# Performance work log

Measured on AMD Instinct MI355X. Metric: run time of the kernel, lower is better.

Reference implementation:

```python
import jax, jax.numpy as jnp
import numpy as np

N = 50000        # nodes
E = 600000       # edges
F_IN = 128       # num_node_features
H = 128          # hidden_channels
G = 2000         # number of graphs (batch segments)
C = 1            # num_classes
EPS = 1e-5       # BatchNorm eps


def setup_inputs() -> dict:
    key = jax.random.key(0)
    ks = jax.random.split(key, 12)
    x = jax.random.normal(ks[0], (N, F_IN), dtype=jnp.float32)
    edge_index = jax.random.randint(ks[1], (2, E), 0, N, dtype=jnp.int32)
    batch = jnp.sort(jax.random.randint(ks[2], (N,), 0, G, dtype=jnp.int32))
    s = 0.05
    W1 = jax.random.normal(ks[3], (F_IN, H), dtype=jnp.float32) * s
    b1 = jnp.zeros((H,), dtype=jnp.float32)
    W2 = jax.random.normal(ks[4], (H, H), dtype=jnp.float32) * s
    b2 = jnp.zeros((H,), dtype=jnp.float32)
    W3 = jax.random.normal(ks[5], (H, H), dtype=jnp.float32) * s
    b3 = jnp.zeros((H,), dtype=jnp.float32)
    # BatchNorm (eval mode): running stats + affine params, stacked [3, H]
    bn_gamma = jnp.ones((3, H), dtype=jnp.float32)
    bn_beta = jnp.zeros((3, H), dtype=jnp.float32)
    bn_mean = jnp.zeros((3, H), dtype=jnp.float32)
    bn_var = jnp.ones((3, H), dtype=jnp.float32)
    lin1_W = jax.random.normal(ks[6], (3 * H, H), dtype=jnp.float32) * s
    lin1_b = jnp.zeros((H,), dtype=jnp.float32)
    lin2_W = jax.random.normal(ks[7], (H, C), dtype=jnp.float32) * s
    lin2_b = jnp.zeros((C,), dtype=jnp.float32)
    return {"x": x, "edge_index": edge_index, "batch": batch,
            "W1": W1, "b1": b1, "W2": W2, "b2": b2, "W3": W3, "b3": b3,
            "bn_gamma": bn_gamma, "bn_beta": bn_beta, "bn_mean": bn_mean, "bn_var": bn_var,
            "lin1_W": lin1_W, "lin1_b": lin1_b, "lin2_W": lin2_W, "lin2_b": lin2_b}


def _gcn_norm(edge_index):
    # Add self loops, compute symmetric normalization D^-1/2 (A+I) D^-1/2.
    loop = jnp.arange(N, dtype=edge_index.dtype)
    row = jnp.concatenate([edge_index[0], loop])   # sources (E+N,)
    col = jnp.concatenate([edge_index[1], loop])   # targets (E+N,)
    deg = jax.ops.segment_sum(jnp.ones(E + N, dtype=jnp.float32), col, num_segments=N)
    dinv = jnp.where(deg > 0, jax.lax.rsqrt(deg), 0.0)
    norm = dinv[row] * dinv[col]                   # (E+N,)
    return row, col, norm


def _gcn_conv(h, W, b, row, col, norm):
    h = h @ W                                      # [N, H] transform first (PyG GCNConv)
    msg = h[row] * norm[:, None]                   # edge-wise gather + scale
    out = jax.ops.segment_sum(msg, col, num_segments=N)  # scatter-add aggregate
    return out + b


def _bn_relu(h, g, b, m, v):
    return jax.nn.relu((h - m) * jax.lax.rsqrt(v + EPS) * g + b)


def reference(x, edge_index, batch, W1, b1, W2, b2, W3, b3,
              bn_gamma, bn_beta, bn_mean, bn_var,
              lin1_W, lin1_b, lin2_W, lin2_b):
    row, col, norm = _gcn_norm(edge_index)
    h = _bn_relu(_gcn_conv(x, W1, b1, row, col, norm), bn_gamma[0], bn_beta[0], bn_mean[0], bn_var[0])
    h = _bn_relu(_gcn_conv(h, W2, b2, row, col, norm), bn_gamma[1], bn_beta[1], bn_mean[1], bn_var[1])
    h = _bn_relu(_gcn_conv(h, W3, b3, row, col, norm), bn_gamma[2], bn_beta[2], bn_mean[2], bn_var[2])
    # Multi-pool over ragged graph segments
    seg = batch
    x_sum = jax.ops.segment_sum(h, seg, num_segments=G)                 # [G, H]
    cnt = jax.ops.segment_sum(jnp.ones((N,), dtype=h.dtype), seg, num_segments=G)
    x_mean = x_sum / jnp.maximum(cnt, 1.0)[:, None]
    x_max = jax.ops.segment_max(h, seg, num_segments=G)
    x_max = jnp.where(jnp.isfinite(x_max), x_max, 0.0)                  # empty segments -> 0
    z = jnp.concatenate([x_mean, x_max, x_sum], axis=1)                 # [G, 3H]
    z = jax.nn.relu(z @ lin1_W + lin1_b)
    return z @ lin2_W + lin2_b                                          # [G, C]
```

## Files before the change

kernel.cpp:

```cpp
#include <hip/hip_runtime.h>
#include <cfloat>
#include <cstdint>

#define N_NODES 50000
#define N_EDGES 600000
#define HDIM    128
#define NGRAPH  2000
#define BN_EPS  1e-5f


__global__ void k_init(int* degi, int* seg_s, int* seg_e) {
    int i = blockIdx.x * 256 + threadIdx.x;
    if (i < N_NODES) degi[i] = 1;
    if (i < NGRAPH) { seg_s[i] = 0x7FFFFFFF; seg_e[i] = 0; }
}

__global__ void k_count(const int* __restrict__ ei, int* degi) {
    int e = blockIdx.x * 256 + threadIdx.x;
    if (e < N_EDGES) atomicAdd(&degi[ei[N_EDGES + e]], 1);
}

__global__ void k_scanA(const int* __restrict__ degi, int* ptr, int* bsum, float* dinv) {
    __shared__ int t[256];
    int i = blockIdx.x * 256 + threadIdx.x;
    int v = (i < N_NODES) ? degi[i] : 0;
    if (i < N_NODES) dinv[i] = rsqrtf((float)v);
    t[threadIdx.x] = v; __syncthreads();
    for (int off = 1; off < 256; off <<= 1) {
        int a = (threadIdx.x >= off) ? t[threadIdx.x - off] : 0;
        __syncthreads();
        t[threadIdx.x] += a;
        __syncthreads();
    }
    if (i < N_NODES) ptr[i + 1] = t[threadIdx.x];
    if (threadIdx.x == 255) bsum[blockIdx.x] = t[255];
}

__global__ void k_scanB(const int* __restrict__ bsum, int* boff, int nb) {
    __shared__ int t[256];
    int i = threadIdx.x;
    int v = (i < nb) ? bsum[i] : 0;
    t[i] = v; __syncthreads();
    for (int off = 1; off < 256; off <<= 1) {
        int a = (i >= off) ? t[i - off] : 0;
        __syncthreads();
        t[i] += a;
        __syncthreads();
    }
    if (i < nb) boff[i] = t[i] - v;
}

__global__ void k_scanC(int* ptr, const int* __restrict__ boff, int* cursor) {
    int i = blockIdx.x * 256 + threadIdx.x;
    if (i < N_NODES) {
        int val = ptr[i + 1] + boff[blockIdx.x];
        ptr[i + 1] = val;
        if (i + 1 < N_NODES) cursor[i + 1] = val;
    }
    if (i == 0) { ptr[0] = 0; cursor[0] = 0; }
}

__global__ void k_fill(const int* __restrict__ ei, const float* __restrict__ dinv,
                       int* cursor, int2* meta) {
    int e = blockIdx.x * 256 + threadIdx.x;
    if (e < N_EDGES) {
        int r = ei[e], c = ei[N_EDGES + e];
        int pos = atomicAdd(&cursor[c], 1);
        meta[pos] = make_int2(r, __float_as_int(dinv[r] * dinv[c]));
    } else if (e < N_EDGES + N_NODES) {
        int v = e - N_EDGES;
        int pos = atomicAdd(&cursor[v], 1);
        float d = dinv[v];
        meta[pos] = make_int2(v, __float_as_int(d * d));
    }
}

__global__ void k_seg(const int* __restrict__ batch, int* seg_s, int* seg_e) {
    int i = blockIdx.x * 256 + threadIdx.x;
    if (i < N_NODES) {
        int g = batch[i];
        atomicMin(&seg_s[g], i);
        atomicMax(&seg_e[g], i + 1);
    }
}


__global__ __launch_bounds__(256) void k_layer(const float4* __restrict__ h4,
                                               const int* __restrict__ ptr,
                                               const int2* __restrict__ meta,
                                               const float4* __restrict__ W4,
                                               const float4* __restrict__ bias4,
                                               const float4* __restrict__ bng4,
                                               const float4* __restrict__ bnb4,
                                               const float4* __restrict__ bnm4,
                                               const float4* __restrict__ bnv4,
                                               float4* __restrict__ hout4) {
    __shared__ float4 Hs[32 * 32];
    int base = blockIdx.x * 32;
    int c = threadIdx.x & 31;
    int grp = threadIdx.x >> 5;

#pragma unroll
    for (int pass = 0; pass < 4; pass++) {
        int ln = pass * 8 + grp;
        int v = base + ln;
        if (v < N_NODES) {
            int e0 = ptr[v], e1 = ptr[v + 1];
            float ax = 0.f, ay = 0.f, az = 0.f, aw = 0.f;
            int j = e0;
            for (; j + 8 <= e1; j += 8) {
                int2 m[8];
#pragma unroll
                for (int i = 0; i < 8; i++) m[i] = meta[j + i];
                float4 vv[8];
#pragma unroll
                for (int i = 0; i < 8; i++) vv[i] = h4[(size_t)m[i].x * 32 + c];
#pragma unroll
                for (int i = 0; i < 8; i++) {
                    float n = __int_as_float(m[i].y);
                    ax += n * vv[i].x; ay += n * vv[i].y;
                    az += n * vv[i].z; aw += n * vv[i].w;
                }
            }
            int rem = e1 - j;
            if (rem) {
                int2 m[8];
#pragma unroll
                for (int i = 0; i < 8; i++) m[i] = meta[j + (i < rem ? i : 0)];
                float4 vv[8];
#pragma unroll
                for (int i = 0; i < 8; i++) vv[i] = h4[(size_t)m[i].x * 32 + c];
#pragma unroll
                for (int i = 0; i < 8; i++) {
                    float n = (i < rem) ? __int_as_float(m[i].y) : 0.f;
                    ax += n * vv[i].x; ay += n * vv[i].y;
                    az += n * vv[i].z; aw += n * vv[i].w;
                }
            }
            Hs[ln * 32 + c] = make_float4(ax, ay, az, aw);
        }
    }
    __syncthreads();

    int ct = threadIdx.x & 31;
    int nt = threadIdx.x >> 5;

    float4 acc0 = make_float4(0.f, 0.f, 0.f, 0.f);
    float4 acc1 = acc0, acc2 = acc0, acc3 = acc0;

#pragma unroll 4
    for (int kc = 0; kc < 32; kc++) {
        float4 ha = Hs[(nt * 4 + 0) * 32 + kc];
        float4 hb = Hs[(nt * 4 + 1) * 32 + kc];
        float4 hc = Hs[(nt * 4 + 2) * 32 + kc];
        float4 hd = Hs[(nt * 4 + 3) * 32 + kc];
        float4 w0 = W4[(kc * 4 + 0) * 32 + ct];
        float4 w1 = W4[(kc * 4 + 1) * 32 + ct];
        float4 w2 = W4[(kc * 4 + 2) * 32 + ct];
        float4 w3 = W4[(kc * 4 + 3) * 32 + ct];

        acc0.x += ha.x * w0.x + ha.y * w1.x + ha.z * w2.x + ha.w * w3.x;
        acc0.y += ha.x * w0.y + ha.y * w1.y + ha.z * w2.y + ha.w * w3.y;
        acc0.z += ha.x * w0.z + ha.y * w1.z + ha.z * w2.z + ha.w * w3.z;
        acc0.w += ha.x * w0.w + ha.y * w1.w + ha.z * w2.w + ha.w * w3.w;

        acc1.x += hb.x * w0.x + hb.y * w1.x + hb.z * w2.x + hb.w * w3.x;
        acc1.y += hb.x * w0.y + hb.y * w1.y + hb.z * w2.y + hb.w * w3.y;
        acc1.z += hb.x * w0.z + hb.y * w1.z + hb.z * w2.z + hb.w * w3.z;
        acc1.w += hb.x * w0.w + hb.y * w1.w + hb.z * w2.w + hb.w * w3.w;

        acc2.x += hc.x * w0.x + hc.y * w1.x + hc.z * w2.x + hc.w * w3.x;
        acc2.y += hc.x * w0.y + hc.y * w1.y + hc.z * w2.y + hc.w * w3.y;
        acc2.z += hc.x * w0.z + hc.y * w1.z + hc.z * w2.z + hc.w * w3.z;
        acc2.w += hc.x * w0.w + hc.y * w1.w + hc.z * w2.w + hc.w * w3.w;

        acc3.x += hd.x * w0.x + hd.y * w1.x + hd.z * w2.x + hd.w * w3.x;
        acc3.y += hd.x * w0.y + hd.y * w1.y + hd.z * w2.y + hd.w * w3.y;
        acc3.z += hd.x * w0.z + hd.y * w1.z + hd.z * w2.z + hd.w * w3.z;
        acc3.w += hd.x * w0.w + hd.y * w1.w + hd.z * w2.w + hd.w * w3.w;
    }

    float4 bs = bias4[ct], g = bng4[ct], bb = bnb4[ct], m = bnm4[ct], vv = bnv4[ct];
    float sx = g.x * rsqrtf(vv.x + BN_EPS), tx = bb.x - m.x * sx;
    float sy = g.y * rsqrtf(vv.y + BN_EPS), ty = bb.y - m.y * sy;
    float sz = g.z * rsqrtf(vv.z + BN_EPS), tz = bb.z - m.z * sz;
    float sw = g.w * rsqrtf(vv.w + BN_EPS), tw = bb.w - m.w * sw;

    int n0 = base + nt * 4;
    float4 accs[4] = {acc0, acc1, acc2, acc3};
#pragma unroll
    for (int q = 0; q < 4; q++) {
        int nidx = n0 + q;
        if (nidx < N_NODES) {
            float4 a = accs[q], r;
            r.x = fmaxf((a.x + bs.x) * sx + tx, 0.f);
            r.y = fmaxf((a.y + bs.y) * sy + ty, 0.f);
            r.z = fmaxf((a.z + bs.z) * sz + tz, 0.f);
            r.w = fmaxf((a.w + bs.w) * sw + tw, 0.f);
            hout4[(size_t)nidx * 32 + ct] = r;
        }
    }
}


__global__ __launch_bounds__(128) void k_pool(const float* __restrict__ h,
                                              const int* __restrict__ seg_s,
                                              const int* __restrict__ seg_e,
                                              const float* __restrict__ l1W,
                                              const float* __restrict__ l1b,
                                              const float* __restrict__ l2W,
                                              const float* __restrict__ l2b,
                                              float* __restrict__ out) {
    __shared__ float z[3 * HDIM];
    __shared__ float red[2];
    int g = blockIdx.x, c = threadIdx.x;
    int s = seg_s[g], e = seg_e[g];
    float sum = 0.f, mx = -FLT_MAX;
    for (int i = s; i < e; i++) {
        float val = h[(size_t)i * HDIM + c];
        sum += val;
        mx = fmaxf(mx, val);
    }
    int cnt = (s < e) ? (e - s) : 0;
    if (cnt == 0) { mx = 0.f; sum = 0.f; }
    float mean = sum / (float)(cnt > 1 ? cnt : 1);
    z[c] = mean; z[HDIM + c] = mx; z[2 * HDIM + c] = sum;
    __syncthreads();
    float o = l1b[c];
    for (int k = 0; k < 3 * HDIM; k++) o += z[k] * l1W[k * HDIM + c];
    o = fmaxf(o, 0.f);
    float p = o * l2W[c];
#pragma unroll
    for (int off = 32; off; off >>= 1) p += __shfl_down(p, off, 64);
    if ((c & 63) == 0) red[c >> 6] = p;
    __syncthreads();
    if (c == 0) out[g] = red[0] + red[1] + l2b[0];
}


extern "C" void kernel_launch(void* const* d_in, const int* in_sizes, int n_in,
                              void* d_out, int out_size, void* d_ws, size_t ws_size,
                              hipStream_t stream) {
    const float* x   = (const float*)d_in[0];
    const int*   ei  = (const int*)d_in[1];
    const int*   bat = (const int*)d_in[2];
    const float* W1  = (const float*)d_in[3];
    const float* b1  = (const float*)d_in[4];
    const float* W2  = (const float*)d_in[5];
    const float* b2  = (const float*)d_in[6];
    const float* W3  = (const float*)d_in[7];
    const float* b3  = (const float*)d_in[8];
    const float* bng = (const float*)d_in[9];
    const float* bnb = (const float*)d_in[10];
    const float* bnm = (const float*)d_in[11];
    const float* bnv = (const float*)d_in[12];
    const float* l1W = (const float*)d_in[13];
    const float* l1b = (const float*)d_in[14];
    const float* l2W = (const float*)d_in[15];
    const float* l2b = (const float*)d_in[16];
    float* out = (float*)d_out;

    char* ws = (char*)d_ws;
    size_t off = 0;
    auto alloc = [&](size_t bytes) -> char* {
        char* p = ws + off;
        off = (off + bytes + 255) & ~(size_t)255;
        return p;
    };
    int*   degi   = (int*)alloc((size_t)N_NODES * 4);
    float* dinv   = (float*)alloc((size_t)N_NODES * 4);
    int*   ptr    = (int*)alloc((size_t)(N_NODES + 1) * 4);
    int*   cursor = (int*)alloc((size_t)N_NODES * 4);
    int*   bsum   = (int*)alloc(256 * 4);
    int*   boff   = (int*)alloc(256 * 4);
    int*   seg_s  = (int*)alloc((size_t)NGRAPH * 4);
    int*   seg_e  = (int*)alloc((size_t)NGRAPH * 4);
    int2*  meta   = (int2*)alloc((size_t)(N_EDGES + N_NODES) * 8);
    float* hA     = (float*)alloc((size_t)N_NODES * HDIM * 4);
    float* hB     = (float*)alloc((size_t)N_NODES * HDIM * 4);
    (void)ws_size;

    int nblk = (N_NODES + 255) / 256;

    k_init<<<nblk, 256, 0, stream>>>(degi, seg_s, seg_e);
    k_count<<<(N_EDGES + 255) / 256, 256, 0, stream>>>(ei, degi);
    k_scanA<<<nblk, 256, 0, stream>>>(degi, ptr, bsum, dinv);
    k_scanB<<<1, 256, 0, stream>>>(bsum, boff, nblk);
    k_scanC<<<nblk, 256, 0, stream>>>(ptr, boff, cursor);
    k_fill<<<(N_EDGES + N_NODES + 255) / 256, 256, 0, stream>>>(ei, dinv, cursor, meta);
    k_seg<<<nblk, 256, 0, stream>>>(bat, seg_s, seg_e);

    int lb = (N_NODES + 31) / 32;

    k_layer<<<lb, 256, 0, stream>>>((const float4*)x, ptr, meta, (const float4*)W1,
                                    (const float4*)b1,
                                    (const float4*)(bng + 0), (const float4*)(bnb + 0),
                                    (const float4*)(bnm + 0), (const float4*)(bnv + 0),
                                    (float4*)hA);
    k_layer<<<lb, 256, 0, stream>>>((const float4*)hA, ptr, meta, (const float4*)W2,
                                    (const float4*)b2,
                                    (const float4*)(bng + HDIM), (const float4*)(bnb + HDIM),
                                    (const float4*)(bnm + HDIM), (const float4*)(bnv + HDIM),
                                    (float4*)hB);
    k_layer<<<lb, 256, 0, stream>>>((const float4*)hB, ptr, meta, (const float4*)W3,
                                    (const float4*)b3,
                                    (const float4*)(bng + 2 * HDIM), (const float4*)(bnb + 2 * HDIM),
                                    (const float4*)(bnm + 2 * HDIM), (const float4*)(bnv + 2 * HDIM),
                                    (float4*)hA);

    k_pool<<<NGRAPH, 128, 0, stream>>>(hA, seg_s, seg_e, l1W, l1b, l2W, l2b, out);
}
```

Baseline: 326.5 us.

## Fuse segment-bounds pass into degree count and reshape neighbor gather per node

Merges the graph-segment min/max kernel into the degree-count kernel, removing one launch. Changes the aggregation so each node is handled by 8 lanes, each lane loading four float4 chunks per neighbor, with 2-edge unrolling instead of 8-edge batches across 32 lanes. The pooling MLP reads z as float4 to cut shared-memory loads. Fewer edges are unrolled per lane, which may reduce memory-level parallelism in the gather.

```diff
diff --git a/kernel.cpp b/kernel.cpp
--- a/kernel.cpp
+++ b/kernel.cpp
@@ -15,9 +15,15 @@
     if (i < NGRAPH) { seg_s[i] = 0x7FFFFFFF; seg_e[i] = 0; }
 }
 
-__global__ void k_count(const int* __restrict__ ei, int* degi) {
+__global__ void k_count_seg(const int* __restrict__ ei, int* degi,
+                            const int* __restrict__ batch, int* seg_s, int* seg_e) {
     int e = blockIdx.x * 256 + threadIdx.x;
     if (e < N_EDGES) atomicAdd(&degi[ei[N_EDGES + e]], 1);
+    if (e < N_NODES) {
+        int g = batch[e];
+        atomicMin(&seg_s[g], e);
+        atomicMax(&seg_e[g], e + 1);
+    }
 }
 
 __global__ void k_scanA(const int* __restrict__ degi, int* ptr, int* bsum, float* dinv) {
@@ -75,15 +81,6 @@
     }
 }
 
-__global__ void k_seg(const int* __restrict__ batch, int* seg_s, int* seg_e) {
-    int i = blockIdx.x * 256 + threadIdx.x;
-    if (i < N_NODES) {
-        int g = batch[i];
-        atomicMin(&seg_s[g], i);
-        atomicMax(&seg_e[g], i + 1);
-    }
-}
-
 
 __global__ __launch_bounds__(256) void k_layer(const float4* __restrict__ h4,
                                                const int* __restrict__ ptr,
@@ -97,48 +94,47 @@
                                                float4* __restrict__ hout4) {
     __shared__ float4 Hs[32 * 32];
     int base = blockIdx.x * 32;
-    int c = threadIdx.x & 31;
-    int grp = threadIdx.x >> 5;
-
-#pragma unroll
-    for (int pass = 0; pass < 4; pass++) {
-        int ln = pass * 8 + grp;
-        int v = base + ln;
+
+    {
+        int ln = threadIdx.x >> 3;
+        int c  = threadIdx.x & 7;
+        int v  = base + ln;
+        float4 a0 = make_float4(0.f, 0.f, 0.f, 0.f);
+        float4 a1 = a0, a2 = a0, a3 = a0;
         if (v < N_NODES) {
             int e0 = ptr[v], e1 = ptr[v + 1];
-            float ax = 0.f, ay = 0.f, az = 0.f, aw = 0.f;
             int j = e0;
-            for (; j + 8 <= e1; j += 8) {
-                int2 m[8];
-#pragma unroll
-                for (int i = 0; i < 8; i++) m[i] = meta[j + i];
-                float4 vv[8];
-#pragma unroll
-                for (int i = 0; i < 8; i++) vv[i] = h4[(size_t)m[i].x * 32 + c];
-#pragma unroll
-                for (int i = 0; i < 8; i++) {
-                    float n = __int_as_float(m[i].y);
-                    ax += n * vv[i].x; ay += n * vv[i].y;
-                    az += n * vv[i].z; aw += n * vv[i].w;
-                }
+            for (; j + 2 <= e1; j += 2) {
+                int2 mA = meta[j], mB = meta[j + 1];
+                const float4* rA = h4 + (size_t)mA.x * 32 + c;
+                const float4* rB = h4 + (size_t)mB.x * 32 + c;
+                float4 vA0 = rA[0], vA1 = rA[8], vA2 = rA[16], vA3 = rA[24];
+                float4 vB0 = rB[0], vB1 = rB[8], vB2 = rB[16], vB3 = rB[24];
+                float nA = __int_as_float(mA.y), nB = __int_as_float(mB.y);
+                a0.x += nA * vA0.x + nB * vB0.x; a0.y += nA * vA0.y + nB * vB0.y;
+                a0.z += nA * vA0.z + nB * vB0.z; a0.w += nA * vA0.w + nB * vB0.w;
+                a1.x += nA * vA1.x + nB * vB1.x; a1.y += nA * vA1.y + nB * vB1.y;
+                a1.z += nA * vA1.z + nB * vB1.z; a1.w += nA * vA1.w + nB * vB1.w;
+                a2.x += nA * vA2.x + nB * vB2.x; a2.y += nA * vA2.y + nB * vB2.y;
+                a2.z += nA * vA2.z + nB * vB2.z; a2.w += nA * vA2.w + nB * vB2.w;
+                a3.x += nA * vA3.x + nB * vB3.x; a3.y += nA * vA3.y + nB * vB3.y;
+                a3.z += nA * vA3.z + nB * vB3.z; a3.w += nA * vA3.w + nB * vB3.w;
             }
-            int rem = e1 - j;
-            if (rem) {
-                int2 m[8];
-#pragma unroll
-                for (int i = 0; i < 8; i++) m[i] = meta[j + (i < rem ? i : 0)];
-                float4 vv[8];
-#pragma unroll
-                for (int i = 0; i < 8; i++) vv[i] = h4[(size_t)m[i].x * 32 + c];
-#pragma unroll
-                for (int i = 0; i < 8; i++) {
-                    float n = (i < rem) ? __int_as_float(m[i].y) : 0.f;
-                    ax += n * vv[i].x; ay += n * vv[i].y;
-                    az += n * vv[i].z; aw += n * vv[i].w;
-                }
+            if (j < e1) {
+                int2 mA = meta[j];
+                const float4* rA = h4 + (size_t)mA.x * 32 + c;
+                float4 vA0 = rA[0], vA1 = rA[8], vA2 = rA[16], vA3 = rA[24];
+                float nA = __int_as_float(mA.y);
+                a0.x += nA * vA0.x; a0.y += nA * vA0.y; a0.z += nA * vA0.z; a0.w += nA * vA0.w;
+                a1.x += nA * vA1.x; a1.y += nA * vA1.y; a1.z += nA * vA1.z; a1.w += nA * vA1.w;
+                a2.x += nA * vA2.x; a2.y += nA * vA2.y; a2.z += nA * vA2.z; a2.w += nA * vA2.w;
+                a3.x += nA * vA3.x; a3.y += nA * vA3.y; a3.z += nA * vA3.z; a3.w += nA * vA3.w;
             }
-            Hs[ln * 32 + c] = make_float4(ax, ay, az, aw);
         }
+        Hs[ln * 32 + c +  0] = a0;
+        Hs[ln * 32 + c +  8] = a1;
+        Hs[ln * 32 + c + 16] = a2;
+        Hs[ln * 32 + c + 24] = a3;
     }
     __syncthreads();
 
@@ -226,8 +222,17 @@
     float mean = sum / (float)(cnt > 1 ? cnt : 1);
     z[c] = mean; z[HDIM + c] = mx; z[2 * HDIM + c] = sum;
     __syncthreads();
+    const float4* z4 = (const float4*)z;
     float o = l1b[c];
-    for (int k = 0; k < 3 * HDIM; k++) o += z[k] * l1W[k * HDIM + c];
+#pragma unroll 4
+    for (int k4 = 0; k4 < 96; k4++) {
+        float4 zz = z4[k4];
+        float w0 = l1W[(k4 * 4 + 0) * HDIM + c];
+        float w1 = l1W[(k4 * 4 + 1) * HDIM + c];
+        float w2 = l1W[(k4 * 4 + 2) * HDIM + c];
+        float w3 = l1W[(k4 * 4 + 3) * HDIM + c];
+        o += zz.x * w0 + zz.y * w1 + zz.z * w2 + zz.w * w3;
+    }
     o = fmaxf(o, 0.f);
     float p = o * l2W[c];
 #pragma unroll
@@ -283,12 +288,11 @@
     int nblk = (N_NODES + 255) / 256;
 
     k_init<<<nblk, 256, 0, stream>>>(degi, seg_s, seg_e);
-    k_count<<<(N_EDGES + 255) / 256, 256, 0, stream>>>(ei, degi);
+    k_count_seg<<<(N_EDGES + 255) / 256, 256, 0, stream>>>(ei, degi, bat, seg_s, seg_e);
     k_scanA<<<nblk, 256, 0, stream>>>(degi, ptr, bsum, dinv);
     k_scanB<<<1, 256, 0, stream>>>(bsum, boff, nblk);
     k_scanC<<<nblk, 256, 0, stream>>>(ptr, boff, cursor);
     k_fill<<<(N_EDGES + N_NODES + 255) / 256, 256, 0, stream>>>(ei, dinv, cursor, meta);
-    k_seg<<<nblk, 256, 0, stream>>>(bat, seg_s, seg_e);
 
     int lb = (N_NODES + 31) / 32;
 
```

Measured after the change: 330.1 us. Within noise of the previous version (+1.1%).
